# Performance work log

Hardware: AMD Instinct MI355X
Metric: run time of the kernel (lower is better)

## Reference

```python
import jax, jax.numpy as jnp
import numpy as np

B, S, D, H = 2, 2048, 1024, 16
DK = D // H  # 64


def setup_inputs() -> dict:
    key = jax.random.key(0)
    ks = jax.random.split(key, 4)
    scale = 1.0 / np.sqrt(D)
    return {
        "q_input": jax.random.normal(ks[0], (B, S, D), dtype=jnp.float32),
        "W_q": jax.random.normal(ks[1], (D, D), dtype=jnp.float32) * scale,
        "b_q": jnp.zeros((D,), dtype=jnp.float32),
        "W_k": jax.random.normal(ks[2], (D, D), dtype=jnp.float32) * scale,
        "b_k": jnp.zeros((D,), dtype=jnp.float32),
        "W_v": jax.random.normal(ks[3], (D, D), dtype=jnp.float32) * scale,
        "b_v": jnp.zeros((D,), dtype=jnp.float32),
    }


def reference(q_input, W_q, b_q, W_k, b_k, W_v, b_v):
    # Self-attention: k_input and v_input default to q_input in the torch module.
    # nn.Linear computes x @ W.T + b
    q = q_input @ W_q.T + b_q
    k = q_input @ W_k.T + b_k
    v = q_input @ W_v.T + b_v

    # [B,S,D] -> [B,H,S,DK]
    def split_heads(x):
        return x.reshape(B, S, H, DK).transpose(0, 2, 1, 3)

    qh, kh, vh = split_heads(q), split_heads(k), split_heads(v)

    # scores [B,H,S,S]; causal mask added BEFORE scaling (as in source; -inf invariant)
    scores = jnp.einsum("bhqd,bhkd->bhqk", qh, kh)
    causal = jnp.tril(jnp.ones((S, S), dtype=bool))
    scores = jnp.where(causal[None, None], scores, -jnp.inf)
    scores = scores / jnp.sqrt(jnp.float32(DK))
    probs = jax.nn.softmax(scores, axis=-1)
    z = jnp.einsum("bhqk,bhkd->bhqd", probs, vh)  # [B,H,S,DK]
    # [B,H,S,DK] -> [B,S,H,DK] -> [B,S,D]
    return z.transpose(0, 2, 1, 3).reshape(B, S, D)
```

## Files before the change

kernel.cpp:

```cpp
#include <hip/hip_runtime.h>
#include <hip/hip_bf16.h>
#include <stdint.h>

typedef __attribute__((ext_vector_type(8))) short short8;
typedef __attribute__((ext_vector_type(4))) short short4v;
typedef __attribute__((ext_vector_type(4))) float f32x4;
typedef __attribute__((ext_vector_type(16))) float f32x16;

#define B_ 2
#define S_ 2048
#define D_ 1024
#define H_ 16
#define DK_ 64
#define M_ (B_*S_)

#define WS_QKV   0
#define WS_XB    12582912
#define WS_WB    16777216

#define QSCALE (0.125f * 1.44269504088896f)

#define GLL16(g, l) __builtin_amdgcn_global_load_lds( \
    (const __attribute__((address_space(1))) void*)(g), \
    (__attribute__((address_space(3))) void*)(l), 16, 0, 0)

#define WAIT_VM0 asm volatile("s_waitcnt vmcnt(0)" ::: "memory")
#define WAIT_VM4 asm volatile("s_waitcnt vmcnt(4)" ::: "memory")
#define WAIT_VM8 asm volatile("s_waitcnt vmcnt(8)" ::: "memory")
#define WAIT_LGKM0 asm volatile("s_waitcnt lgkmcnt(0)" ::: "memory")
#define BARRIER_RAW asm volatile("s_barrier" ::: "memory")

static __device__ __forceinline__ short f2bf(float f){
  union { float f; unsigned u; } x; x.f = f;
  unsigned r = x.u + 0x7fff + ((x.u >> 16) & 1);
  return (short)(r >> 16);
}

__global__ __launch_bounds__(256) void cvt_bf16(
    const float* __restrict__ X,  const float* __restrict__ Wq,
    const float* __restrict__ Wk, const float* __restrict__ Wv,
    short* __restrict__ ws)
{
  const int z = blockIdx.z;
  const float* src; short* dst; int n;
  if (z == 0)      { src = X;  dst = ws + WS_XB;               n = M_*D_; }
  else if (z == 1) { src = Wq; dst = ws + WS_WB;               n = D_*D_; }
  else if (z == 2) { src = Wk; dst = ws + WS_WB + D_*D_;       n = D_*D_; }
  else             { src = Wv; dst = ws + WS_WB + 2*(D_*D_);   n = D_*D_; }
  const int stride = gridDim.x * blockDim.x * 4;
  for (int i = (blockIdx.x * blockDim.x + threadIdx.x) * 4; i < n; i += stride) {
    float4 v = *(const float4*)(src + i);
    short4v o;
    o.x = f2bf(v.x); o.y = f2bf(v.y); o.z = f2bf(v.z); o.w = f2bf(v.w);
    *(short4v*)(dst + i) = o;
  }
}

__global__ __launch_bounds__(512, 2) void qkv_gemm(
    const short* __restrict__ ws_in,
    const float* __restrict__ bq, const float* __restrict__ bk,
    const float* __restrict__ bv, short* __restrict__ qkv)
{
  const int z = blockIdx.z;
  const short* X  = ws_in + WS_XB;
  const short* Wm = ws_in + WS_WB + (size_t)z * (D_*D_);
  short* out = qkv + (size_t)z * (M_*D_);

  __shared__ __align__(16) short lds[65536];

  const int t = threadIdx.x;
  const int w = t >> 6, lane = t & 63;
  const int quad = lane >> 4, l16 = lane & 15;
  const int wm = w >> 2, wn = w & 3;
  const int m0 = blockIdx.y * 256, n0 = blockIdx.x * 256;

  const int rl = t >> 2;
  const int sl = (t & 3) ^ (rl & 3);
  const short* sA0 = X  + (size_t)(m0 + rl) * D_ + sl*8;
  const short* sA1 = sA0 + (size_t)128 * D_;
  const short* sB0 = Wm + (size_t)(n0 + rl) * D_ + sl*8;
  const short* sB1 = sB0 + (size_t)128 * D_;
  const int ldsw = w << 9;

  const int swz = quad ^ (l16 & 3);

  f32x4 acc[8][4];
  #pragma unroll
  for (int i=0;i<8;i++)
    #pragma unroll
    for (int j=0;j<4;j++) acc[i][j] = (f32x4){0.f,0.f,0.f,0.f};

  #pragma unroll
  for (int p=0;p<3;p++){
    GLL16(sA0 + p*32, lds + p*16384 + ldsw);
    GLL16(sA1 + p*32, lds + p*16384 + 4096 + ldsw);
    GLL16(sB0 + p*32, lds + p*16384 + 8192 + ldsw);
    GLL16(sB1 + p*32, lds + p*16384 + 12288 + ldsw);
  }
  WAIT_VM8;
  BARRIER_RAW;

  for (int kt = 0; kt < 32; kt++) {
    const int bf = kt & 3;
    const short* bufA = lds + bf*16384;
    const short* bufB = bufA + 8192;
    const int tb = (kt + 3) & 3;
    const int ko2 = (kt + 3) * 32;
    const bool st = (kt + 3) < 32;

    short8 aF[4], bF[4];
    #pragma unroll
    for (int mf=0; mf<4; mf++)
      aF[mf] = *(const short8*)(bufA + (wm*128 + mf*16 + l16)*32 + swz*8);
    #pragma unroll
    for (int nf=0; nf<4; nf++)
      bF[nf] = *(const short8*)(bufB + (wn*64 + nf*16 + l16)*32 + swz*8);
    if (st) {
      GLL16(sA0 + ko2, lds + tb*16384 + ldsw);
      GLL16(sA1 + ko2, lds + tb*16384 + 4096 + ldsw);
    }
    BARRIER_RAW;
    WAIT_LGKM0;
    __builtin_amdgcn_s_setprio(1);
    #pragma unroll
    for (int mf=0; mf<4; mf++)
      #pragma unroll
      for (int nf=0; nf<4; nf++)
        acc[mf][nf] = __builtin_amdgcn_mfma_f32_16x16x32_bf16(aF[mf], bF[nf], acc[mf][nf], 0,0,0);
    __builtin_amdgcn_s_setprio(0);
    BARRIER_RAW;

    #pragma unroll
    for (int mf=0; mf<4; mf++)
      aF[mf] = *(const short8*)(bufA + (wm*128 + 64 + mf*16 + l16)*32 + swz*8);
    if (st) {
      GLL16(sB0 + ko2, lds + tb*16384 + 8192 + ldsw);
      GLL16(sB1 + ko2, lds + tb*16384 + 12288 + ldsw);
    }
    BARRIER_RAW;
    WAIT_LGKM0;
    __builtin_amdgcn_s_setprio(1);
    #pragma unroll
    for (int mf=0; mf<4; mf++)
      #pragma unroll
      for (int nf=0; nf<4; nf++)
        acc[4+mf][nf] = __builtin_amdgcn_mfma_f32_16x16x32_bf16(aF[mf], bF[nf], acc[4+mf][nf], 0,0,0);
    __builtin_amdgcn_s_setprio(0);
    if      (kt < 29)  { WAIT_VM8; }
    else if (kt == 29) { WAIT_VM4; }
    else if (kt == 30) { WAIT_VM0; }
    BARRIER_RAW;
  }

  __syncthreads();

  if (z != 2) {
    const float scale = (z==0) ? QSCALE : 1.0f;
    const float* bias = (z==0) ? bq : bk;
    float bv4[4];
    #pragma unroll
    for (int nf=0; nf<4; nf++) bv4[nf] = bias[n0 + wn*64 + nf*16 + l16];
    short* ep = lds;
    #pragma unroll
    for (int p=0; p<2; p++){
      if (wm == p){
        #pragma unroll
        for (int mf=0; mf<8; mf++)
          #pragma unroll
          for (int nf=0; nf<4; nf++)
            #pragma unroll
            for (int i=0; i<4; i++)
              ep[(mf*16 + quad*4 + i)*264 + wn*64 + nf*16 + l16] =
                  f2bf((acc[mf][nf][i] + bv4[nf]) * scale);
      }
      __syncthreads();
      #pragma unroll
      for (int it=0; it<8; it++){
        const int cid = it*512 + t;
        const int row = cid >> 5, cc = cid & 31;
        short8 vv = *(const short8*)(ep + row*264 + cc*8);
        const int m = m0 + p*128 + row, bidx = m >> 11, s = m & 2047;
        const int n = n0 + cc*8, h = n >> 6, dd = n & 63;
        *(short8*)(out + (((size_t)(bidx*H_ + h))*S_ + s)*DK_ + dd) = vv;
      }
      __syncthreads();
    }
  } else {
    float bv4[4];
    #pragma unroll
    for (int nf=0; nf<4; nf++) bv4[nf] = bv[n0 + wn*64 + nf*16 + l16];
    short* ep = lds;
    #pragma unroll
    for (int p=0; p<2; p++){
      if (wm == p){
        #pragma unroll
        for (int mf=0; mf<8; mf++)
          #pragma unroll
          for (int nf=0; nf<4; nf++)
            #pragma unroll
            for (int i=0; i<4; i++)
              ep[(wn*64 + nf*16 + l16)*136 + mf*16 + quad*4 + i] =
                  f2bf(acc[mf][nf][i] + bv4[nf]);
      }
      __syncthreads();
      #pragma unroll
      for (int it=0; it<8; it++){
        const int cid = it*512 + t;
        const int row = cid >> 4, cc = cid & 15;
        short8 vv = *(const short8*)(ep + row*136 + cc*8);
        const int n = n0 + row, h = n >> 6, dd = n & 63;
        const int m0p = m0 + p*128;
        const int bidx = m0p >> 11;
        const int s = (m0p & 2047) + cc*8;
        *(short8*)(out + (((size_t)(bidx*H_ + h))*DK_ + dd)*S_ + s) = vv;
      }
      __syncthreads();
    }
  }
}

__global__ __launch_bounds__(512, 2) void attn(
    const short* __restrict__ qkv, float* __restrict__ out)
{
  const int bh = blockIdx.y;
  const int qt = 7 - blockIdx.x;
  const short* Q  = qkv + (size_t)bh * (S_*DK_);
  const short* K  = Q + (size_t)(M_*D_);
  const short* VT = qkv + (size_t)(2*M_*D_) + (size_t)bh * (DK_*S_);

  __shared__ short Kbuf[2][4096];
  __shared__ short Vbuf[2][4096];

  const int t = threadIdx.x;
  const int w = t >> 6, lane = t & 63;
  const int l32 = lane & 31, h = lane >> 5;

  const int q0w = qt*256 + w*32;

  short8 bq[4];
  #pragma unroll
  for (int dc=0; dc<4; dc++)
    bq[dc] = *(const short8*)(Q + (size_t)(q0w + l32)*DK_ + dc*16 + h*8);

  const int sr  = w*8 + (lane >> 3);
  const int sc8 = ((lane & 7) ^ (lane >> 3)) * 8;

  const int nkt = 4*(qt+1);
  GLL16(K  + (size_t)sr*DK_ + sc8, &Kbuf[0][0] + w*512);
  GLL16(VT + (size_t)sr*S_  + sc8, &Vbuf[0][0] + w*512);

  f32x16 o0 = {0.f,0.f,0.f,0.f,0.f,0.f,0.f,0.f,0.f,0.f,0.f,0.f,0.f,0.f,0.f,0.f};
  f32x16 o1 = o0;
  float lsum = 0.f;
  const int xrow = l32 & 7;

  for (int kt = 0; kt < nkt; kt++){
    const int cur = kt & 1;
    WAIT_VM0;
    BARRIER_RAW;
    if (kt + 1 < nkt) {
      const int kb2 = (kt+1)*64;
      GLL16(K  + (size_t)(kb2 + sr)*DK_ + sc8, &Kbuf[cur^1][0] + w*512);
      GLL16(VT + (size_t)sr*S_ + kb2 + sc8,    &Vbuf[cur^1][0] + w*512);
    }
    const int kb = kt*64;
    if (kb > q0w + 31) continue;

    const short* Kc = &Kbuf[cur][0];
    const short* Vc = &Vbuf[cur][0];

    f32x16 s[2];
    s[0] = o0 - o0;
    s[1] = s[0];
    #pragma unroll
    for (int dc=0; dc<4; dc++){
      const int xk = ((dc*2 + h) ^ xrow)*8;
      short8 a0 = *(const short8*)(Kc + l32*64 + xk);
      short8 a1 = *(const short8*)(Kc + (32 + l32)*64 + xk);
      s[0] = __builtin_amdgcn_mfma_f32_32x32x16_bf16(a0, bq[dc], s[0], 0,0,0);
      s[1] = __builtin_amdgcn_mfma_f32_32x32x16_bf16(a1, bq[dc], s[1], 0,0,0);
    }

    if (kb + 63 > q0w) {
      const int qg = q0w + l32;
      #pragma unroll
      for (int r=0; r<16; r++){
        const int k0 = kb + (r&3) + 8*(r>>2) + 4*h;
        if (k0      > qg) s[0][r] = -3.0e38f;
        if (k0 + 32 > qg) s[1][r] = -3.0e38f;
      }
    }

    short8 pf[4];
    #pragma unroll
    for (int mk=0; mk<2; mk++){
      #pragma unroll
      for (int u=0; u<2; u++){
        float p0 = __builtin_amdgcn_exp2f(s[mk][8*u+0]);
        float p1 = __builtin_amdgcn_exp2f(s[mk][8*u+1]);
        float p2 = __builtin_amdgcn_exp2f(s[mk][8*u+2]);
        float p3 = __builtin_amdgcn_exp2f(s[mk][8*u+3]);
        float p4 = __builtin_amdgcn_exp2f(s[mk][8*u+4]);
        float p5 = __builtin_amdgcn_exp2f(s[mk][8*u+5]);
        float p6 = __builtin_amdgcn_exp2f(s[mk][8*u+6]);
        float p7 = __builtin_amdgcn_exp2f(s[mk][8*u+7]);
        lsum += ((p0+p1)+(p2+p3)) + ((p4+p5)+(p6+p7));
        unsigned X0, X1, Y0, Y1;
        asm("v_cvt_pk_bf16_f32 %0, %1, %2" : "=v"(X0) : "v"(p0), "v"(p1));
        asm("v_cvt_pk_bf16_f32 %0, %1, %2" : "=v"(X1) : "v"(p2), "v"(p3));
        asm("v_cvt_pk_bf16_f32 %0, %1, %2" : "=v"(Y0) : "v"(p4), "v"(p5));
        asm("v_cvt_pk_bf16_f32 %0, %1, %2" : "=v"(Y1) : "v"(p6), "v"(p7));
        asm("v_permlane32_swap_b32 %0, %1" : "+v"(X0), "+v"(Y0));
        asm("v_permlane32_swap_b32 %0, %1" : "+v"(X1), "+v"(Y1));
        union { unsigned u4[4]; short8 s8; } pp;
        pp.u4[0] = X0; pp.u4[1] = X1; pp.u4[2] = Y0; pp.u4[3] = Y1;
        pf[mk*2 + u] = pp.s8;
      }
    }

    #pragma unroll
    for (int kk=0; kk<4; kk++){
      const int xv = ((kk*2 + h) ^ xrow)*8;
      short8 v0 = *(const short8*)(Vc + l32*64 + xv);
      short8 v1 = *(const short8*)(Vc + (32 + l32)*64 + xv);
      o0 = __builtin_amdgcn_mfma_f32_32x32x16_bf16(pf[kk], v0, o0, 0,0,0);
      o1 = __builtin_amdgcn_mfma_f32_32x32x16_bf16(pf[kk], v1, o1, 0,0,0);
    }
  }

  float rs = lsum + __shfl_xor(lsum, 32, 64);
  float linv = 1.0f / rs;
  const int bb = bh >> 4, hh = bh & 15;
  #pragma unroll
  for (int r=0; r<16; r++){
    const int qrow = (r&3) + 8*(r>>2) + 4*h;
    const float lw = __shfl(linv, qrow, 64);
    const int qg = q0w + qrow;
    float* dst = out + ((size_t)bb*S_ + qg)*D_ + hh*DK_;
    dst[l32]      = o0[r] * lw;
    dst[32 + l32] = o1[r] * lw;
  }
}

extern "C" void kernel_launch(void* const* d_in, const int* in_sizes, int n_in,
                              void* d_out, int out_size, void* d_ws, size_t ws_size,
                              hipStream_t stream)
{
  (void)in_sizes; (void)n_in; (void)out_size; (void)ws_size;
  const float* X  = (const float*)d_in[0];
  const float* Wq = (const float*)d_in[1];
  const float* bq = (const float*)d_in[2];
  const float* Wk = (const float*)d_in[3];
  const float* bk = (const float*)d_in[4];
  const float* Wv = (const float*)d_in[5];
  const float* bv = (const float*)d_in[6];
  short* ws  = (short*)d_ws;
  float* out = (float*)d_out;

  dim3 g0(1024, 1, 4);
  cvt_bf16<<<g0, dim3(256,1,1), 0, stream>>>(X, Wq, Wk, Wv, ws);
  dim3 g1(D_/256, M_/256, 3);
  qkv_gemm<<<g1, dim3(512,1,1), 0, stream>>>(ws, bq, bk, bv, ws + WS_QKV);
  dim3 g2(8, B_*H_);
  attn<<<g2, dim3(512,1,1), 0, stream>>>(ws + WS_QKV, out);
}
```

Baseline: 175.2 us.

## Pair early and late causal query tiles per block with triple-buffered K/V

Each attention block now handles two 128-row query tiles, one early and one late (p and 15-p), so every block runs the same 34 K/V tiles and causal work is balanced. The grid becomes 256 blocks of 256 threads. K/V loading moves to a three-stage global-to-LDS pipeline with prefetch distance 3, and K and V fragments are read into registers before the barrier. This targets load imbalance and tail effects from the triangular workload and tries to hide load latency, at the cost of more registers and LDS and occupancy limited to one block per launch-bound setting.

```diff
diff --git a/kernel.cpp b/kernel.cpp
--- a/kernel.cpp
+++ b/kernel.cpp
@@ -219,126 +219,186 @@
   }
 }
 
-__global__ __launch_bounds__(512, 2) void attn(
+__global__ __launch_bounds__(256, 1) void attn(
     const short* __restrict__ qkv, float* __restrict__ out)
 {
-  const int bh = blockIdx.y;
-  const int qt = 7 - blockIdx.x;
+  const int id = blockIdx.x;
+  const int slot = id >> 3;
+  const int bh = (id & 7) + 8*(slot & 3);
+  const int p  = slot >> 2;
+  const int nA = 2*p + 2;
+
   const short* Q  = qkv + (size_t)bh * (S_*DK_);
   const short* K  = Q + (size_t)(M_*D_);
   const short* VT = qkv + (size_t)(2*M_*D_) + (size_t)bh * (DK_*S_);
 
-  __shared__ short Kbuf[2][4096];
-  __shared__ short Vbuf[2][4096];
+  __shared__ short Kbuf[3][4096];
+  __shared__ short Vbuf[3][4096];
 
   const int t = threadIdx.x;
   const int w = t >> 6, lane = t & 63;
   const int l32 = lane & 31, h = lane >> 5;
-
-  const int q0w = qt*256 + w*32;
-
-  short8 bq[4];
+  const int xrow = l32 & 7;
+
+  const int qA0 = p*128 + w*32;
+  const int qB0 = (15-p)*128 + w*32;
+
+  short8 bqA[4], bqB[4];
   #pragma unroll
-  for (int dc=0; dc<4; dc++)
-    bq[dc] = *(const short8*)(Q + (size_t)(q0w + l32)*DK_ + dc*16 + h*8);
-
-  const int sr  = w*8 + (lane >> 3);
-  const int sc8 = ((lane & 7) ^ (lane >> 3)) * 8;
-
-  const int nkt = 4*(qt+1);
-  GLL16(K  + (size_t)sr*DK_ + sc8, &Kbuf[0][0] + w*512);
-  GLL16(VT + (size_t)sr*S_  + sc8, &Vbuf[0][0] + w*512);
+  for (int dc=0; dc<4; dc++){
+    bqA[dc] = *(const short8*)(Q + (size_t)(qA0 + l32)*DK_ + dc*16 + h*8);
+    bqB[dc] = *(const short8*)(Q + (size_t)(qB0 + l32)*DK_ + dc*16 + h*8);
+  }
+  #pragma unroll
+  for (int dc=0; dc<4; dc++){
+    asm volatile("" : "+v"(bqA[dc]));
+    asm volatile("" : "+v"(bqB[dc]));
+  }
+
+  const int r8   = lane >> 3;
+  const int sc8  = ((lane & 7) ^ r8) * 8;
+  const int row0 = w*16 + r8;
+
+  #pragma unroll
+  for (int pt=0; pt<3; pt++){
+    const int kb = (pt < nA ? pt : pt - nA) * 64;
+    #pragma unroll
+    for (int j=0; j<2; j++){
+      GLL16(K  + (size_t)(kb + row0 + j*8)*DK_ + sc8, &Kbuf[pt][0] + w*1024 + j*512);
+      GLL16(VT + (size_t)(row0 + j*8)*S_ + kb + sc8,  &Vbuf[pt][0] + w*1024 + j*512);
+    }
+  }
+  WAIT_VM8;
+  BARRIER_RAW;
 
   f32x16 o0 = {0.f,0.f,0.f,0.f,0.f,0.f,0.f,0.f,0.f,0.f,0.f,0.f,0.f,0.f,0.f,0.f};
   f32x16 o1 = o0;
   float lsum = 0.f;
-  const int xrow = l32 & 7;
-
-  for (int kt = 0; kt < nkt; kt++){
-    const int cur = kt & 1;
-    WAIT_VM0;
-    BARRIER_RAW;
-    if (kt + 1 < nkt) {
-      const int kb2 = (kt+1)*64;
-      GLL16(K  + (size_t)(kb2 + sr)*DK_ + sc8, &Kbuf[cur^1][0] + w*512);
-      GLL16(VT + (size_t)sr*S_ + kb2 + sc8,    &Vbuf[cur^1][0] + w*512);
-    }
-    const int kb = kt*64;
-    if (kb > q0w + 31) continue;
-
+  const int bb = bh >> 4, hh = bh & 15;
+
+  int cur = 0;
+  for (int ft = 0; ft < 34; ft++){
+    const bool segB = ft >= nA;
+    const int kb   = (segB ? ft - nA : ft) * 64;
+    const int q0w  = segB ? qB0 : qA0;
+    const bool active = (kb <= q0w + 31);
     const short* Kc = &Kbuf[cur][0];
     const short* Vc = &Vbuf[cur][0];
 
-    f32x16 s[2];
-    s[0] = o0 - o0;
-    s[1] = s[0];
-    #pragma unroll
-    for (int dc=0; dc<4; dc++){
-      const int xk = ((dc*2 + h) ^ xrow)*8;
-      short8 a0 = *(const short8*)(Kc + l32*64 + xk);
-      short8 a1 = *(const short8*)(Kc + (32 + l32)*64 + xk);
-      s[0] = __builtin_amdgcn_mfma_f32_32x32x16_bf16(a0, bq[dc], s[0], 0,0,0);
-      s[1] = __builtin_amdgcn_mfma_f32_32x32x16_bf16(a1, bq[dc], s[1], 0,0,0);
-    }
-
-    if (kb + 63 > q0w) {
-      const int qg = q0w + l32;
+    short8 ak[8], vk[8];
+    if (active){
+      #pragma unroll
+      for (int dc=0; dc<4; dc++){
+        const int xk = ((dc*2 + h) ^ xrow)*8;
+        ak[dc]   = *(const short8*)(Kc + l32*64 + xk);
+        ak[4+dc] = *(const short8*)(Kc + (32 + l32)*64 + xk);
+        vk[dc]   = *(const short8*)(Vc + l32*64 + xk);
+        vk[4+dc] = *(const short8*)(Vc + (32 + l32)*64 + xk);
+      }
+    }
+    WAIT_LGKM0;
+    BARRIER_RAW;
+
+    if (ft + 3 < 34){
+      const int f3 = ft + 3;
+      const int kbp = (f3 < nA ? f3 : f3 - nA) * 64;
+      #pragma unroll
+      for (int j=0; j<2; j++){
+        GLL16(K  + (size_t)(kbp + row0 + j*8)*DK_ + sc8, &Kbuf[cur][0] + w*1024 + j*512);
+        GLL16(VT + (size_t)(row0 + j*8)*S_ + kbp + sc8,  &Vbuf[cur][0] + w*1024 + j*512);
+      }
+    }
+
+    if (active){
+      f32x16 s[2];
+      s[0] = o0 - o0;
+      s[1] = s[0];
+      #pragma unroll
+      for (int dc=0; dc<4; dc++){
+        const short8 bqv = segB ? bqB[dc] : bqA[dc];
+        s[0] = __builtin_amdgcn_mfma_f32_32x32x16_bf16(ak[dc],   bqv, s[0], 0,0,0);
+        s[1] = __builtin_amdgcn_mfma_f32_32x32x16_bf16(ak[4+dc], bqv, s[1], 0,0,0);
+      }
+
+      if (kb + 63 > q0w) {
+        const int qg = q0w + l32;
+        #pragma unroll
+        for (int r=0; r<16; r++){
+          const int k0 = kb + (r&3) + 8*(r>>2) + 4*h;
+          if (k0      > qg) s[0][r] = -3.0e38f;
+          if (k0 + 32 > qg) s[1][r] = -3.0e38f;
+        }
+      }
+
+      short8 pf[4];
+      #pragma unroll
+      for (int mk=0; mk<2; mk++){
+        #pragma unroll
+        for (int u=0; u<2; u++){
+          float p0 = __builtin_amdgcn_exp2f(s[mk][8*u+0]);
+          float p1 = __builtin_amdgcn_exp2f(s[mk][8*u+1]);
+          float p2 = __builtin_amdgcn_exp2f(s[mk][8*u+2]);
+          float p3 = __builtin_amdgcn_exp2f(s[mk][8*u+3]);
+          float p4 = __builtin_amdgcn_exp2f(s[mk][8*u+4]);
+          float p5 = __builtin_amdgcn_exp2f(s[mk][8*u+5]);
+          float p6 = __builtin_amdgcn_exp2f(s[mk][8*u+6]);
+          float p7 = __builtin_amdgcn_exp2f(s[mk][8*u+7]);
+          lsum += ((p0+p1)+(p2+p3)) + ((p4+p5)+(p6+p7));
+          unsigned X0, X1, Y0, Y1;
+          asm("v_cvt_pk_bf16_f32 %0, %1, %2" : "=v"(X0) : "v"(p0), "v"(p1));
+          asm("v_cvt_pk_bf16_f32 %0, %1, %2" : "=v"(X1) : "v"(p2), "v"(p3));
+          asm("v_cvt_pk_bf16_f32 %0, %1, %2" : "=v"(Y0) : "v"(p4), "v"(p5));
+          asm("v_cvt_pk_bf16_f32 %0, %1, %2" : "=v"(Y1) : "v"(p6), "v"(p7));
+          asm("v_permlane32_swap_b32 %0, %1" : "+v"(X0), "+v"(Y0));
+          asm("v_permlane32_swap_b32 %0, %1" : "+v"(X1), "+v"(Y1));
+          union { unsigned u4[4]; short8 s8; } pp;
+          pp.u4[0] = X0; pp.u4[1] = X1; pp.u4[2] = Y0; pp.u4[3] = Y1;
+          pf[mk*2 + u] = pp.s8;
+        }
+      }
+
+      #pragma unroll
+      for (int kk=0; kk<4; kk++){
+        o0 = __builtin_amdgcn_mfma_f32_32x32x16_bf16(pf[kk], vk[kk],   o0, 0,0,0);
+        o1 = __builtin_amdgcn_mfma_f32_32x32x16_bf16(pf[kk], vk[4+kk], o1, 0,0,0);
+      }
+    }
+
+    if (ft == nA - 1){
+      float rs = lsum + __shfl_xor(lsum, 32, 64);
+      float linv = 1.0f / rs;
       #pragma unroll
       for (int r=0; r<16; r++){
-        const int k0 = kb + (r&3) + 8*(r>>2) + 4*h;
-        if (k0      > qg) s[0][r] = -3.0e38f;
-        if (k0 + 32 > qg) s[1][r] = -3.0e38f;
-      }
-    }
-
-    short8 pf[4];
-    #pragma unroll
-    for (int mk=0; mk<2; mk++){
-      #pragma unroll
-      for (int u=0; u<2; u++){
-        float p0 = __builtin_amdgcn_exp2f(s[mk][8*u+0]);
-        float p1 = __builtin_amdgcn_exp2f(s[mk][8*u+1]);
-        float p2 = __builtin_amdgcn_exp2f(s[mk][8*u+2]);
-        float p3 = __builtin_amdgcn_exp2f(s[mk][8*u+3]);
-        float p4 = __builtin_amdgcn_exp2f(s[mk][8*u+4]);
-        float p5 = __builtin_amdgcn_exp2f(s[mk][8*u+5]);
-        float p6 = __builtin_amdgcn_exp2f(s[mk][8*u+6]);
-        float p7 = __builtin_amdgcn_exp2f(s[mk][8*u+7]);
-        lsum += ((p0+p1)+(p2+p3)) + ((p4+p5)+(p6+p7));
-        unsigned X0, X1, Y0, Y1;
-        asm("v_cvt_pk_bf16_f32 %0, %1, %2" : "=v"(X0) : "v"(p0), "v"(p1));
-        asm("v_cvt_pk_bf16_f32 %0, %1, %2" : "=v"(X1) : "v"(p2), "v"(p3));
-        asm("v_cvt_pk_bf16_f32 %0, %1, %2" : "=v"(Y0) : "v"(p4), "v"(p5));
-        asm("v_cvt_pk_bf16_f32 %0, %1, %2" : "=v"(Y1) : "v"(p6), "v"(p7));
-        asm("v_permlane32_swap_b32 %0, %1" : "+v"(X0), "+v"(Y0));
-        asm("v_permlane32_swap_b32 %0, %1" : "+v"(X1), "+v"(Y1));
-        union { unsigned u4[4]; short8 s8; } pp;
-        pp.u4[0] = X0; pp.u4[1] = X1; pp.u4[2] = Y0; pp.u4[3] = Y1;
-        pf[mk*2 + u] = pp.s8;
-      }
-    }
-
-    #pragma unroll
-    for (int kk=0; kk<4; kk++){
-      const int xv = ((kk*2 + h) ^ xrow)*8;
-      short8 v0 = *(const short8*)(Vc + l32*64 + xv);
-      short8 v1 = *(const short8*)(Vc + (32 + l32)*64 + xv);
-      o0 = __builtin_amdgcn_mfma_f32_32x32x16_bf16(pf[kk], v0, o0, 0,0,0);
-      o1 = __builtin_amdgcn_mfma_f32_32x32x16_bf16(pf[kk], v1, o1, 0,0,0);
-    }
-  }
-
-  float rs = lsum + __shfl_xor(lsum, 32, 64);
-  float linv = 1.0f / rs;
-  const int bb = bh >> 4, hh = bh & 15;
-  #pragma unroll
-  for (int r=0; r<16; r++){
-    const int qrow = (r&3) + 8*(r>>2) + 4*h;
-    const float lw = __shfl(linv, qrow, 64);
-    const int qg = q0w + qrow;
-    float* dst = out + ((size_t)bb*S_ + qg)*D_ + hh*DK_;
-    dst[l32]      = o0[r] * lw;
-    dst[32 + l32] = o1[r] * lw;
+        const int qrow = (r&3) + 8*(r>>2) + 4*h;
+        const float lw = __shfl(linv, qrow, 64);
+        float* dst = out + ((size_t)bb*S_ + (qA0 + qrow))*D_ + hh*DK_;
+        dst[l32]      = o0[r] * lw;
+        dst[32 + l32] = o1[r] * lw;
+      }
+      o0 = o0 - o0; o1 = o1 - o1; lsum = 0.f;
+    }
+
+    {
+      const int rem = 33 - ft;
+      if      (rem >= 3) { WAIT_VM8; }
+      else if (rem == 2) { WAIT_VM4; }
+      else if (rem == 1) { WAIT_VM0; }
+    }
+    BARRIER_RAW;
+    cur = (cur == 2) ? 0 : cur + 1;
+  }
+
+  {
+    float rs = lsum + __shfl_xor(lsum, 32, 64);
+    float linv = 1.0f / rs;
+    #pragma unroll
+    for (int r=0; r<16; r++){
+      const int qrow = (r&3) + 8*(r>>2) + 4*h;
+      const float lw = __shfl(linv, qrow, 64);
+      float* dst = out + ((size_t)bb*S_ + (qB0 + qrow))*D_ + hh*DK_;
+      dst[l32]      = o0[r] * lw;
+      dst[32 + l32] = o1[r] * lw;
+    }
   }
 }
 
@@ -361,6 +421,6 @@
   cvt_bf16<<<g0, dim3(256,1,1), 0, stream>>>(X, Wq, Wk, Wv, ws);
   dim3 g1(D_/256, M_/256, 3);
   qkv_gemm<<<g1, dim3(512,1,1), 0, stream>>>(ws, bq, bk, bv, ws + WS_QKV);
-  dim3 g2(8, B_*H_);
-  attn<<<g2, dim3(512,1,1), 0, stream>>>(ws + WS_QKV, out);
+  dim3 g2(256, 1);
+  attn<<<g2, dim3(256,1,1), 0, stream>>>(ws + WS_QKV, out);
 }
```

After: 177.2 us. About the same (+1.1%).
